# Optimization experiments

Measured on AMD Instinct MI355X. Metric: run time of the kernel, lower is better.

Reference implementation:

```python
import jax, jax.numpy as jnp
import numpy as np
from jax import lax

EPS = 1e-5

def quantize_ternary(w):
    # scale = mean(|w|).clamp_min(1e-5) computed on detached weight
    scale = jnp.maximum(jnp.mean(jnp.abs(lax.stop_gradient(w))), EPS)
    ws = w / scale
    # STE: forward uses round+clamp, backward is identity in ws
    wq = lax.stop_gradient(jnp.clip(jnp.round(ws), -1.0, 1.0) - ws) + ws
    return wq * scale

def conv2d(x, w, b):
    # x: [N,C,H,W], w: [O,I,kh,kw], stride 1, pad 1 -> same spatial size
    out = lax.conv_general_dilated(
        x, w, window_strides=(1, 1), padding=[(1, 1), (1, 1)],
        dimension_numbers=("NCHW", "OIHW", "NCHW"))
    return out + b[None, :, None, None]

def setup_inputs() -> dict:
    key = jax.random.key(0)
    k1, k2, k3, k4, k5 = jax.random.split(key, 5)
    N, C_in, C_out, H, W, K = 16, 64, 64, 128, 128, 3
    fan_in = C_in * K * K
    bound = 1.0 / np.sqrt(fan_in)
    x = jax.random.normal(k1, (N, C_in, H, W), dtype=jnp.float32)
    w = jax.random.uniform(k2, (C_out, C_in, K, K), minval=-bound, maxval=bound, dtype=jnp.float32)
    b = jax.random.uniform(k3, (C_out,), minval=-bound, maxval=bound, dtype=jnp.float32)
    # growth child: kaiming-uniform-like init scaled by 0.01, zero bias
    w_child = jax.random.uniform(k4, (C_out, C_in, K, K), minval=-bound, maxval=bound, dtype=jnp.float32) * 0.01
    b_child = jnp.zeros((C_out,), dtype=jnp.float32)
    gate = jnp.zeros((1,), dtype=jnp.float32)  # growth_gate buffer
    return {"x": x, "w": w, "b": b, "w_child": w_child, "b_child": b_child, "gate": gate}

def reference(x, w, b, w_child, b_child, gate):
    out = conv2d(x, quantize_ternary(w), b)
    child_out = conv2d(x, quantize_ternary(w_child), b_child)
    g = jax.nn.sigmoid(gate)  # shape [1], broadcasts
    return out + g * child_out
```

## Files before the change

### kernel.cpp

```cpp
#include <hip/hip_runtime.h>
#include <math.h>


typedef __attribute__((ext_vector_type(8))) short short8;
typedef __attribute__((ext_vector_type(4))) float float4v;

__device__ inline unsigned short f2bf(float f) {
  union { float f; unsigned u; } v; v.f = f;
  unsigned u = v.u;
  return (unsigned short)((u + 0x7FFFu + ((u >> 16) & 1u)) >> 16);
}

__global__ __launch_bounds__(256) void prep(
    const float* __restrict__ w, const float* __restrict__ wc,
    const float* __restrict__ b, const float* __restrict__ bc,
    const float* __restrict__ gate,
    unsigned short* __restrict__ wq, float* __restrict__ beff) {
  const int tid = threadIdx.x;
  const float4v* w4 = (const float4v*)w;
  const float4v* c4 = (const float4v*)wc;
  double a0 = 0, a1 = 0, a2 = 0, a3 = 0;
  double c0 = 0, c1 = 0, c2 = 0, c3 = 0;
#pragma unroll
  for (int i = 0; i < 36; i += 4) {
    float4v wa = w4[tid + (i + 0) * 256];
    float4v wb = w4[tid + (i + 1) * 256];
    float4v wcv = w4[tid + (i + 2) * 256];
    float4v wd = w4[tid + (i + 3) * 256];
    float4v xa = c4[tid + (i + 0) * 256];
    float4v xb = c4[tid + (i + 1) * 256];
    float4v xc = c4[tid + (i + 2) * 256];
    float4v xd = c4[tid + (i + 3) * 256];
    a0 += (double)fabsf(wa[0]) + (double)fabsf(wa[1]) + (double)fabsf(wa[2]) + (double)fabsf(wa[3]);
    a1 += (double)fabsf(wb[0]) + (double)fabsf(wb[1]) + (double)fabsf(wb[2]) + (double)fabsf(wb[3]);
    a2 += (double)fabsf(wcv[0]) + (double)fabsf(wcv[1]) + (double)fabsf(wcv[2]) + (double)fabsf(wcv[3]);
    a3 += (double)fabsf(wd[0]) + (double)fabsf(wd[1]) + (double)fabsf(wd[2]) + (double)fabsf(wd[3]);
    c0 += (double)fabsf(xa[0]) + (double)fabsf(xa[1]) + (double)fabsf(xa[2]) + (double)fabsf(xa[3]);
    c1 += (double)fabsf(xb[0]) + (double)fabsf(xb[1]) + (double)fabsf(xb[2]) + (double)fabsf(xb[3]);
    c2 += (double)fabsf(xc[0]) + (double)fabsf(xc[1]) + (double)fabsf(xc[2]) + (double)fabsf(xc[3]);
    c3 += (double)fabsf(xd[0]) + (double)fabsf(xd[1]) + (double)fabsf(xd[2]) + (double)fabsf(xd[3]);
  }
  double a = (a0 + a1) + (a2 + a3);
  double c = (c0 + c1) + (c2 + c3);
#pragma unroll
  for (int off = 32; off > 0; off >>= 1) {
    a += __shfl_down(a, off);
    c += __shfl_down(c, off);
  }
  __shared__ double sa[4], sc[4];
  const int wv = tid >> 6;
  if ((tid & 63) == 0) { sa[wv] = a; sc[wv] = c; }
  __syncthreads();
  const double ta = (sa[0] + sa[1]) + (sa[2] + sa[3]);
  const double tc = (sc[0] + sc[1]) + (sc[2] + sc[3]);
  const float sw = fmaxf((float)(ta * (1.0 / 36864.0)), 1e-5f);
  const float scl = fmaxf((float)(tc * (1.0 / 36864.0)), 1e-5f);
  const float g = 1.0f / (1.0f + expf(-gate[0]));
  const int idx = blockIdx.x * 256 + tid;
  const int tap = idx >> 12;
  const int oc = (idx >> 6) & 63;
  const int ci = idx & 63;
  const int src = oc * 576 + ci * 9 + tap;
  float q1 = fminf(1.f, fmaxf(-1.f, rintf(w[src] / sw))) * sw;
  float q2 = fminf(1.f, fmaxf(-1.f, rintf(wc[src] / scl))) * scl;
  wq[idx] = f2bf(q1 + g * q2);
  if (idx < 64) beff[idx] = b[idx] + g * bc[idx];
}

__global__ __launch_bounds__(256, 2) void conv_fused(
    const float* __restrict__ x, const unsigned short* __restrict__ wq,
    const float* __restrict__ beff, float* __restrict__ out) {
  extern __shared__ __align__(16) char smem[];
  char* Abase = smem;
  char* Bbase = smem + 65536;

  const int bid = blockIdx.x;
  const int xcd = bid & 7;
  const int u = bid >> 3;
  const int n = xcd * 2 + (u >> 6);
  const int h0 = (u & 63) * 2;
  const int tid = threadIdx.x;
  const int lane = tid & 63;
  const int wv = tid >> 6;
  const int rw = wv >> 1;
  const int pxh = (wv & 1) * 64;
  const int ln15 = lane & 15;
  const int lq = lane >> 4;

  const float* xn = x + (size_t)n * (64 * 16384);

  const short8 b0a = *(const short8*)(wq + tid * 16);
  const short8 b0b = *(const short8*)(wq + tid * 16 + 8);

  const int pxc = tid & 127;
  const int hi = tid >> 7;
#pragma unroll
  for (int grp = 0; grp < 4; ++grp) {
    float t[4][8];
#pragma unroll
    for (int j = 0; j < 4; ++j) {
      const int k = grp * 8 + j * 2 + hi;
      const int r = k >> 3;
      const int c = k & 7;
      const int h = h0 + r - 1;
      if ((unsigned)h < 128u) {
        const float* sp = xn + c * 8 * 16384 + h * 128 + pxc;
#pragma unroll
        for (int e = 0; e < 8; ++e) t[j][e] = sp[e * 16384];
      } else {
#pragma unroll
        for (int e = 0; e < 8; ++e) t[j][e] = 0.f;
      }
    }
#pragma unroll
    for (int j = 0; j < 4; ++j) {
      const int k = grp * 8 + j * 2 + hi;
      const int r = k >> 3;
      const int c = k & 7;
      short8 v;
#pragma unroll
      for (int e = 0; e < 8; ++e) v[e] = (short)f2bf(t[j][e]);
      const int slot = ((r * 128 + pxc) << 3) + (c ^ ((pxc + 1) & 7));
      *(short8*)(Abase + (slot << 4)) = v;
    }
  }

  const int g0 = tid * 2;
  const int oc0 = g0 >> 3;
  const int c0 = g0 & 7;
  const int bs0 = (oc0 << 3) + (c0 ^ (oc0 & 7));
  const int bs1 = (oc0 << 3) + ((c0 + 1) ^ (oc0 & 7));
  *(short8*)(Bbase + (bs0 << 4)) = b0a;
  *(short8*)(Bbase + (bs1 << 4)) = b0b;
  __syncthreads();

  float4v acc[4][4] = {};

#pragma unroll
  for (int tap = 0; tap < 9; ++tap) {
    const int dh = tap / 3;
    const int dw = tap - dh * 3;
    const int r = rw + dh;
    const int pb = pxh + ln15 + dw;
    const bool p0 = (pb == 0);
    const bool p129 = (pb == 81);
    const int a0 = (((r * 128 + pb - 1) << 3) + (lq ^ (pb & 7))) << 4;
    const int off0 = p0 ? 2048 : 0;
    const int off3 = p129 ? 4096 : 6144;

    short8 Ab[2][4], Bb[2][4];
#pragma unroll
    for (int cc = 0; cc < 2; ++cc) {
      const int ax = a0 ^ (cc << 6);
      Ab[cc][0] = *(const short8*)(Abase + (ax + off0));
      Ab[cc][1] = *(const short8*)(Abase + (ax + 2048));
      Ab[cc][2] = *(const short8*)(Abase + (ax + 4096));
      Ab[cc][3] = *(const short8*)(Abase + (ax + off3));
      if (p0) Ab[cc][0] = (short8)0;
      if (p129) Ab[cc][3] = (short8)0;
    }
#pragma unroll
    for (int qd = 0; qd < 4; ++qd) {
      const int oc8 = ((qd << 4) + ln15) << 3;
      const int k7 = ln15 & 7;
      Bb[0][qd] = *(const short8*)(Bbase + ((oc8 + (lq ^ k7)) << 4));
      Bb[1][qd] = *(const short8*)(Bbase + ((oc8 + ((lq + 4) ^ k7)) << 4));
    }

    if (tap < 8) __syncthreads();

    short8 bta, btb;
    if (tap < 8) {
      bta = *(const short8*)(wq + (tap + 1) * 4096 + tid * 16);
      btb = *(const short8*)(wq + (tap + 1) * 4096 + tid * 16 + 8);
    }

    __builtin_amdgcn_s_setprio(1);
#pragma unroll
    for (int cc2 = 0; cc2 < 2; ++cc2)
#pragma unroll
      for (int mf = 0; mf < 4; ++mf)
#pragma unroll
        for (int qd = 0; qd < 4; ++qd)
          acc[mf][qd] = __builtin_amdgcn_mfma_f32_16x16x32_bf16(
              Ab[cc2][mf], Bb[cc2][qd], acc[mf][qd], 0, 0, 0);
    __builtin_amdgcn_s_setprio(0);

    if (tap < 8) {
      *(short8*)(Bbase + (bs0 << 4)) = bta;
      *(short8*)(Bbase + (bs1 << 4)) = btb;
      __syncthreads();
    }
  }

  const int rq = lane >> 4;
  float bias[4];
#pragma unroll
  for (int q = 0; q < 4; ++q) bias[q] = beff[q * 16 + ln15];
#pragma unroll
  for (int mf = 0; mf < 4; ++mf) {
#pragma unroll
    for (int qd = 0; qd < 4; ++qd) {
      float4v v = acc[mf][qd] + bias[qd];
      int oc = qd * 16 + ln15;
      float* op = out + (((n * 64 + oc) * 128 + h0 + rw) * 128 + pxh + mf * 16 + rq * 4);
      *(float4v*)op = v;
    }
  }
}

extern "C" void kernel_launch(void* const* d_in, const int* in_sizes, int n_in,
                              void* d_out, int out_size, void* d_ws, size_t ws_size,
                              hipStream_t stream) {
  const float* x = (const float*)d_in[0];
  const float* w = (const float*)d_in[1];
  const float* b = (const float*)d_in[2];
  const float* wc = (const float*)d_in[3];
  const float* bc = (const float*)d_in[4];
  const float* gate = (const float*)d_in[5];

  unsigned short* wq = (unsigned short*)d_ws;
  float* beff = (float*)((char*)d_ws + 73728);

  prep<<<144, 256, 0, stream>>>(w, wc, b, bc, gate, wq, beff);
  conv_fused<<<1024, 256, 73728, stream>>>(x, wq, beff, (float*)d_out);
}
```

Before: 144.0 us.

## Double block to 512 threads, splitting output channels across wave pairs

Each block now runs 8 waves instead of 4, with wave pairs splitting the 64 output channels into two halves of 32. This halves the accumulators and B fragments per wave, and spreads the x staging and weight-tap loads over more threads. The aim is more latency hiding and lower register pressure per wave. In exchange, each A fragment read from LDS is now loaded by two waves, and every barrier synchronises twice as many waves.

New measurement: 143.2 us. About the same (-0.5%).

```diff
diff --git a/kernel.cpp b/kernel.cpp
--- a/kernel.cpp
+++ b/kernel.cpp
@@ -67,7 +67,7 @@
   if (idx < 64) beff[idx] = b[idx] + g * bc[idx];
 }
 
-__global__ __launch_bounds__(256, 2) void conv_fused(
+__global__ __launch_bounds__(512, 4) void conv_fused(
     const float* __restrict__ x, const unsigned short* __restrict__ wq,
     const float* __restrict__ beff, float* __restrict__ out) {
   extern __shared__ __align__(16) char smem[];
@@ -82,24 +82,24 @@
   const int tid = threadIdx.x;
   const int lane = tid & 63;
   const int wv = tid >> 6;
-  const int rw = wv >> 1;
-  const int pxh = (wv & 1) * 64;
+  const int rw = wv >> 2;
+  const int pxh = ((wv >> 1) & 1) * 64;
+  const int och = (wv & 1) * 32;
   const int ln15 = lane & 15;
   const int lq = lane >> 4;
 
   const float* xn = x + (size_t)n * (64 * 16384);
 
-  const short8 b0a = *(const short8*)(wq + tid * 16);
-  const short8 b0b = *(const short8*)(wq + tid * 16 + 8);
+  const short8 b0v = *(const short8*)(wq + tid * 8);
 
   const int pxc = tid & 127;
   const int hi = tid >> 7;
 #pragma unroll
-  for (int grp = 0; grp < 4; ++grp) {
+  for (int grp = 0; grp < 2; ++grp) {
     float t[4][8];
 #pragma unroll
     for (int j = 0; j < 4; ++j) {
-      const int k = grp * 8 + j * 2 + hi;
+      const int k = grp * 16 + j * 4 + hi;
       const int r = k >> 3;
       const int c = k & 7;
       const int h = h0 + r - 1;
@@ -114,7 +114,7 @@
     }
 #pragma unroll
     for (int j = 0; j < 4; ++j) {
-      const int k = grp * 8 + j * 2 + hi;
+      const int k = grp * 16 + j * 4 + hi;
       const int r = k >> 3;
       const int c = k & 7;
       short8 v;
@@ -125,16 +125,13 @@
     }
   }
 
-  const int g0 = tid * 2;
-  const int oc0 = g0 >> 3;
-  const int c0 = g0 & 7;
+  const int oc0 = tid >> 3;
+  const int c0 = tid & 7;
   const int bs0 = (oc0 << 3) + (c0 ^ (oc0 & 7));
-  const int bs1 = (oc0 << 3) + ((c0 + 1) ^ (oc0 & 7));
-  *(short8*)(Bbase + (bs0 << 4)) = b0a;
-  *(short8*)(Bbase + (bs1 << 4)) = b0b;
+  *(short8*)(Bbase + (bs0 << 4)) = b0v;
   __syncthreads();
 
-  float4v acc[4][4] = {};
+  float4v acc[4][2] = {};
 
 #pragma unroll
   for (int tap = 0; tap < 9; ++tap) {
@@ -148,7 +145,7 @@
     const int off0 = p0 ? 2048 : 0;
     const int off3 = p129 ? 4096 : 6144;
 
-    short8 Ab[2][4], Bb[2][4];
+    short8 Ab[2][4], Bb[2][2];
 #pragma unroll
     for (int cc = 0; cc < 2; ++cc) {
       const int ax = a0 ^ (cc << 6);
@@ -160,8 +157,8 @@
       if (p129) Ab[cc][3] = (short8)0;
     }
 #pragma unroll
-    for (int qd = 0; qd < 4; ++qd) {
-      const int oc8 = ((qd << 4) + ln15) << 3;
+    for (int qd = 0; qd < 2; ++qd) {
+      const int oc8 = (och + (qd << 4) + ln15) << 3;
       const int k7 = ln15 & 7;
       Bb[0][qd] = *(const short8*)(Bbase + ((oc8 + (lq ^ k7)) << 4));
       Bb[1][qd] = *(const short8*)(Bbase + ((oc8 + ((lq + 4) ^ k7)) << 4));
@@ -169,11 +166,8 @@
 
     if (tap < 8) __syncthreads();
 
-    short8 bta, btb;
-    if (tap < 8) {
-      bta = *(const short8*)(wq + (tap + 1) * 4096 + tid * 16);
-      btb = *(const short8*)(wq + (tap + 1) * 4096 + tid * 16 + 8);
-    }
+    short8 btv;
+    if (tap < 8) btv = *(const short8*)(wq + (tap + 1) * 4096 + tid * 8);
 
     __builtin_amdgcn_s_setprio(1);
 #pragma unroll
@@ -181,28 +175,27 @@
 #pragma unroll
       for (int mf = 0; mf < 4; ++mf)
 #pragma unroll
-        for (int qd = 0; qd < 4; ++qd)
+        for (int qd = 0; qd < 2; ++qd)
           acc[mf][qd] = __builtin_amdgcn_mfma_f32_16x16x32_bf16(
               Ab[cc2][mf], Bb[cc2][qd], acc[mf][qd], 0, 0, 0);
     __builtin_amdgcn_s_setprio(0);
 
     if (tap < 8) {
-      *(short8*)(Bbase + (bs0 << 4)) = bta;
-      *(short8*)(Bbase + (bs1 << 4)) = btb;
+      *(short8*)(Bbase + (bs0 << 4)) = btv;
       __syncthreads();
     }
   }
 
   const int rq = lane >> 4;
-  float bias[4];
-#pragma unroll
-  for (int q = 0; q < 4; ++q) bias[q] = beff[q * 16 + ln15];
+  float bias[2];
+#pragma unroll
+  for (int q = 0; q < 2; ++q) bias[q] = beff[och + q * 16 + ln15];
 #pragma unroll
   for (int mf = 0; mf < 4; ++mf) {
 #pragma unroll
-    for (int qd = 0; qd < 4; ++qd) {
+    for (int qd = 0; qd < 2; ++qd) {
       float4v v = acc[mf][qd] + bias[qd];
-      int oc = qd * 16 + ln15;
+      int oc = och + qd * 16 + ln15;
       float* op = out + (((n * 64 + oc) * 128 + h0 + rw) * 128 + pxh + mf * 16 + rq * 4);
       *(float4v*)op = v;
     }
@@ -223,5 +216,5 @@
   float* beff = (float*)((char*)d_ws + 73728);
 
   prep<<<144, 256, 0, stream>>>(w, wc, b, bc, gate, wq, beff);
-  conv_fused<<<1024, 256, 73728, stream>>>(x, wq, beff, (float*)d_out);
-}
+  conv_fused<<<1024, 512, 73728, stream>>>(x, wq, beff, (float*)d_out);
+}
```

## Split input channels into two phases to halve LDS and raise occupancy

Applied to the files above, without the earlier changes.

The conv kernel now stages input channels in two halves of 32 and accumulates across both phases. This halves shared memory per block (72KB to 36KB) and raises launch bounds to 4 blocks per CU, so more waves can hide global load latency. In exchange, each block does two staging passes with extra barriers, and the per-tap B reload is smaller but happens twice as often.

Measured after the change: 170.0 us. 18.1% more time.

```diff
diff --git a/kernel.cpp b/kernel.cpp
--- a/kernel.cpp
+++ b/kernel.cpp
@@ -67,12 +67,12 @@
   if (idx < 64) beff[idx] = b[idx] + g * bc[idx];
 }
 
-__global__ __launch_bounds__(256, 2) void conv_fused(
+__global__ __launch_bounds__(256, 4) void conv_fused(
     const float* __restrict__ x, const unsigned short* __restrict__ wq,
     const float* __restrict__ beff, float* __restrict__ out) {
   extern __shared__ __align__(16) char smem[];
   char* Abase = smem;
-  char* Bbase = smem + 65536;
+  char* Bbase = smem + 32768;
 
   const int bid = blockIdx.x;
   const int xcd = bid & 7;
@@ -89,107 +89,104 @@
 
   const float* xn = x + (size_t)n * (64 * 16384);
 
-  const short8 b0a = *(const short8*)(wq + tid * 16);
-  const short8 b0b = *(const short8*)(wq + tid * 16 + 8);
+  const int oc0 = tid >> 2;
+  const int c0 = tid & 3;
+  const int bslot = ((oc0 ^ ((oc0 >> 2) & 1)) << 2) + (c0 ^ (oc0 & 3));
+  const unsigned short* bsrc = wq + oc0 * 64 + c0 * 8;
+
+  int brd[4];
+#pragma unroll
+  for (int qd = 0; qd < 4; ++qd) {
+    const int oc = qd * 16 + ln15;
+    brd[qd] = (((oc ^ ((oc >> 2) & 1)) << 2) + (lq ^ (oc & 3))) << 4;
+  }
 
   const int pxc = tid & 127;
   const int hi = tid >> 7;
-#pragma unroll
-  for (int grp = 0; grp < 4; ++grp) {
-    float t[4][8];
-#pragma unroll
-    for (int j = 0; j < 4; ++j) {
-      const int k = grp * 8 + j * 2 + hi;
-      const int r = k >> 3;
-      const int c = k & 7;
-      const int h = h0 + r - 1;
-      if ((unsigned)h < 128u) {
-        const float* sp = xn + c * 8 * 16384 + h * 128 + pxc;
-#pragma unroll
-        for (int e = 0; e < 8; ++e) t[j][e] = sp[e * 16384];
-      } else {
-#pragma unroll
-        for (int e = 0; e < 8; ++e) t[j][e] = 0.f;
+
+  float4v acc[4][4] = {};
+
+#pragma unroll
+  for (int ph = 0; ph < 2; ++ph) {
+    const short8 b0 = *(const short8*)(bsrc + ph * 32);
+
+#pragma unroll
+    for (int grp = 0; grp < 2; ++grp) {
+      float t[4][8];
+#pragma unroll
+      for (int j = 0; j < 4; ++j) {
+        const int k = grp * 8 + j * 2 + hi;
+        const int r = k >> 2;
+        const int c = k & 3;
+        const int h = h0 + r - 1;
+        if ((unsigned)h < 128u) {
+          const float* sp = xn + (ph * 32 + c * 8) * 16384 + h * 128 + pxc;
+#pragma unroll
+          for (int e = 0; e < 8; ++e) t[j][e] = sp[e * 16384];
+        } else {
+#pragma unroll
+          for (int e = 0; e < 8; ++e) t[j][e] = 0.f;
+        }
+      }
+#pragma unroll
+      for (int j = 0; j < 4; ++j) {
+        const int k = grp * 8 + j * 2 + hi;
+        const int r = k >> 2;
+        const int c = k & 3;
+        short8 v;
+#pragma unroll
+        for (int e = 0; e < 8; ++e) v[e] = (short)f2bf(t[j][e]);
+        const int row = r * 128 + pxc;
+        const int slot = ((row ^ ((row >> 2) & 1)) << 2) + (c ^ ((pxc + 1) & 3));
+        *(short8*)(Abase + (slot << 4)) = v;
       }
     }
-#pragma unroll
-    for (int j = 0; j < 4; ++j) {
-      const int k = grp * 8 + j * 2 + hi;
-      const int r = k >> 3;
-      const int c = k & 7;
-      short8 v;
-#pragma unroll
-      for (int e = 0; e < 8; ++e) v[e] = (short)f2bf(t[j][e]);
-      const int slot = ((r * 128 + pxc) << 3) + (c ^ ((pxc + 1) & 7));
-      *(short8*)(Abase + (slot << 4)) = v;
-    }
-  }
-
-  const int g0 = tid * 2;
-  const int oc0 = g0 >> 3;
-  const int c0 = g0 & 7;
-  const int bs0 = (oc0 << 3) + (c0 ^ (oc0 & 7));
-  const int bs1 = (oc0 << 3) + ((c0 + 1) ^ (oc0 & 7));
-  *(short8*)(Bbase + (bs0 << 4)) = b0a;
-  *(short8*)(Bbase + (bs1 << 4)) = b0b;
-  __syncthreads();
-
-  float4v acc[4][4] = {};
-
-#pragma unroll
-  for (int tap = 0; tap < 9; ++tap) {
-    const int dh = tap / 3;
-    const int dw = tap - dh * 3;
-    const int r = rw + dh;
-    const int pb = pxh + ln15 + dw;
-    const bool p0 = (pb == 0);
-    const bool p129 = (pb == 81);
-    const int a0 = (((r * 128 + pb - 1) << 3) + (lq ^ (pb & 7))) << 4;
-    const int off0 = p0 ? 2048 : 0;
-    const int off3 = p129 ? 4096 : 6144;
-
-    short8 Ab[2][4], Bb[2][4];
-#pragma unroll
-    for (int cc = 0; cc < 2; ++cc) {
-      const int ax = a0 ^ (cc << 6);
-      Ab[cc][0] = *(const short8*)(Abase + (ax + off0));
-      Ab[cc][1] = *(const short8*)(Abase + (ax + 2048));
-      Ab[cc][2] = *(const short8*)(Abase + (ax + 4096));
-      Ab[cc][3] = *(const short8*)(Abase + (ax + off3));
-      if (p0) Ab[cc][0] = (short8)0;
-      if (p129) Ab[cc][3] = (short8)0;
-    }
-#pragma unroll
-    for (int qd = 0; qd < 4; ++qd) {
-      const int oc8 = ((qd << 4) + ln15) << 3;
-      const int k7 = ln15 & 7;
-      Bb[0][qd] = *(const short8*)(Bbase + ((oc8 + (lq ^ k7)) << 4));
-      Bb[1][qd] = *(const short8*)(Bbase + ((oc8 + ((lq + 4) ^ k7)) << 4));
-    }
-
-    if (tap < 8) __syncthreads();
-
-    short8 bta, btb;
-    if (tap < 8) {
-      bta = *(const short8*)(wq + (tap + 1) * 4096 + tid * 16);
-      btb = *(const short8*)(wq + (tap + 1) * 4096 + tid * 16 + 8);
-    }
-
-    __builtin_amdgcn_s_setprio(1);
-#pragma unroll
-    for (int cc2 = 0; cc2 < 2; ++cc2)
+    *(short8*)(Bbase + (bslot << 4)) = b0;
+    __syncthreads();
+
+#pragma unroll
+    for (int tap = 0; tap < 9; ++tap) {
+      const int dh = tap / 3;
+      const int dw = tap - dh * 3;
+      const int r = rw + dh;
+      const int pb = pxh + ln15 + dw;
+      const bool p0 = (pb == 0);
+      const bool p129 = (pb == 81);
+      const int row = r * 128 + pb - 1;
+      const int row2 = row ^ ((row >> 2) & 1);
+      const int a0 = ((row2 << 2) + (lq ^ (pb & 3))) << 4;
+      const int off0 = p0 ? 1024 : 0;
+      const int off3 = p129 ? 0 : 3072;
+
+      short8 Ab[4], Bb[4];
+      Ab[0] = *(const short8*)(Abase + (a0 + off0));
+      Ab[1] = *(const short8*)(Abase + (a0 + 1024));
+      Ab[2] = *(const short8*)(Abase + (a0 + 2048));
+      Ab[3] = *(const short8*)(Abase + (a0 + off3));
+      if (p0) Ab[0] = (short8)0;
+      if (p129) Ab[3] = (short8)0;
+#pragma unroll
+      for (int qd = 0; qd < 4; ++qd)
+        Bb[qd] = *(const short8*)(Bbase + brd[qd]);
+
+      __syncthreads();
+
+      short8 bnxt;
+      if (tap < 8) bnxt = *(const short8*)(bsrc + (tap + 1) * 4096 + ph * 32);
+
+      __builtin_amdgcn_s_setprio(1);
 #pragma unroll
       for (int mf = 0; mf < 4; ++mf)
 #pragma unroll
         for (int qd = 0; qd < 4; ++qd)
           acc[mf][qd] = __builtin_amdgcn_mfma_f32_16x16x32_bf16(
-              Ab[cc2][mf], Bb[cc2][qd], acc[mf][qd], 0, 0, 0);
-    __builtin_amdgcn_s_setprio(0);
-
-    if (tap < 8) {
-      *(short8*)(Bbase + (bs0 << 4)) = bta;
-      *(short8*)(Bbase + (bs1 << 4)) = btb;
-      __syncthreads();
+              Ab[mf], Bb[qd], acc[mf][qd], 0, 0, 0);
+      __builtin_amdgcn_s_setprio(0);
+
+      if (tap < 8) {
+        *(short8*)(Bbase + (bslot << 4)) = bnxt;
+        __syncthreads();
+      }
     }
   }
 
@@ -223,5 +220,5 @@
   float* beff = (float*)((char*)d_ws + 73728);
 
   prep<<<144, 256, 0, stream>>>(w, wc, b, bc, gate, wq, beff);
-  conv_fused<<<1024, 256, 73728, stream>>>(x, wq, beff, (float*)d_out);
-}
+  conv_fused<<<1024, 256, 36864, stream>>>(x, wq, beff, (float*)d_out);
+}
```
